# Optimization experiments

Hardware: AMD Instinct MI355X
Metric: run time of the kernel (lower is better)

Reference implementation:

```python
import jax, jax.numpy as jnp
import numpy as np

DIM = 128      # link_state_dim
E = 100000     # num edges
P = 800000     # num adjacency pairs
G = 1000       # num graphs
T = 8          # message passing steps
R = 256        # readout_units


def setup_inputs() -> dict:
    key = jax.random.key(0)
    ks = jax.random.split(key, 16)
    s = lambda *shp: 1.0 / np.sqrt(shp[0])
    inp = {
        "link_state": jax.random.normal(ks[0], (E, DIM), dtype=jnp.float32),
        "states_graph_ids": jnp.sort(jax.random.randint(ks[1], (E,), 0, G, dtype=jnp.int32)),
        "states_first": jax.random.randint(ks[2], (P,), 0, E, dtype=jnp.int32),
        "states_second": jax.random.randint(ks[3], (P,), 0, E, dtype=jnp.int32),
        "sates_num_edges": E,
        # Message MLP: Dense(2*DIM -> DIM), selu
        "W_msg": jax.random.normal(ks[4], (2 * DIM, DIM), dtype=jnp.float32) * s(2 * DIM),
        "b_msg": jnp.zeros((DIM,), dtype=jnp.float32),
        # GRUCell (keras default reset_after=True): kernel/recurrent_kernel [DIM, 3*DIM], bias [2, 3*DIM]
        "gru_kernel": jax.random.normal(ks[5], (DIM, 3 * DIM), dtype=jnp.float32) * s(DIM),
        "gru_rec_kernel": jax.random.normal(ks[6], (DIM, 3 * DIM), dtype=jnp.float32) * s(DIM),
        "gru_bias": jnp.zeros((2, 3 * DIM), dtype=jnp.float32),
        # Readout MLP: DIM -> R -> R -> 1
        "W1": jax.random.normal(ks[7], (DIM, R), dtype=jnp.float32) * s(DIM),
        "b1": jnp.zeros((R,), dtype=jnp.float32),
        "W2": jax.random.normal(ks[8], (R, R), dtype=jnp.float32) * s(R),
        "b2": jnp.zeros((R,), dtype=jnp.float32),
        "W3": jax.random.normal(ks[9], (R, 1), dtype=jnp.float32) * s(R),
        "b3": jnp.zeros((1,), dtype=jnp.float32),
    }
    return inp


def _gru_cell(x, h, kernel, rec_kernel, bias):
    # Keras GRUCell, reset_after=True, gate order (z, r, h)
    mx = x @ kernel + bias[0]
    mh = h @ rec_kernel + bias[1]
    xz, xr, xh = jnp.split(mx, 3, axis=1)
    rz, rr, rh = jnp.split(mh, 3, axis=1)
    z = jax.nn.sigmoid(xz + rz)
    r = jax.nn.sigmoid(xr + rr)
    hh = jnp.tanh(xh + r * rh)
    return z * h + (1.0 - z) * hh


def reference(link_state, states_graph_ids, states_first, states_second, sates_num_edges,
              W_msg, b_msg, gru_kernel, gru_rec_kernel, gru_bias,
              W1, b1, W2, b2, W3, b3):
    for _ in range(T):
        # gather main & neighbor edge states, concat on feature dim -> [P, 2*DIM]
        edges_concat = jnp.concatenate([link_state[states_first], link_state[states_second]], axis=1)
        msgs = jax.nn.selu(edges_concat @ W_msg + b_msg)              # [P, DIM]
        agg = jax.ops.segment_sum(msgs, states_second, num_segments=sates_num_edges)  # [E, DIM]
        link_state = _gru_cell(agg, link_state, gru_kernel, gru_rec_kernel, gru_bias)
    pooled = jax.ops.segment_sum(link_state, states_graph_ids, num_segments=G)  # [G, DIM]
    h = jax.nn.selu(pooled @ W1 + b1)
    h = jax.nn.selu(h @ W2 + b2)
    return h @ W3 + b3  # [G, 1]
```

## Files before the change

### kernel.cpp

```cpp
#include <hip/hip_runtime.h>
#include <hip/hip_fp16.h>
#include <math.h>

#define DIM 128
#define E_NUM 100000
#define P_NUM 800000
#define G_NUM 1000
#define T_STEPS 8
#define R_UNITS 256

typedef __attribute__((ext_vector_type(8))) short bf16x8;
typedef __attribute__((ext_vector_type(4))) float f32x4;

typedef unsigned short ushort_t;
typedef unsigned int   uint_t;

__device__ __forceinline__ float selu_f(float x) {
    const float alpha = 1.6732632423543772f;
    const float scale = 1.0507009873554805f;
    return x > 0.f ? scale * x : scale * alpha * expm1f(x);
}

__device__ __forceinline__ float selu_fast(float x) {
    const float scale = 1.0507009873554805f;
    const float A     = 1.7580993408473766f;
    const float l2e   = 1.4426950408889634f;
    const float e = __builtin_amdgcn_exp2f(x * l2e);
    return x > 0.f ? scale * x : A * e - A;
}

__device__ __forceinline__ ushort_t f2bf(float x) {
    uint_t u = __float_as_uint(x);
    uint_t r = (u + 0x7fffu + ((u >> 16) & 1u)) >> 16;
    return (ushort_t)r;
}
__device__ __forceinline__ float bf2f(ushort_t h) {
    return __uint_as_float(((uint_t)h) << 16);
}

__global__ __launch_bounds__(256)
void hist_kernel(const int* __restrict__ second, int* __restrict__ counts)
{
    const int p = blockIdx.x * 256 + threadIdx.x;
    atomicAdd(&counts[second[p]], 1);
}

__global__ __launch_bounds__(1024)
void scanA_kernel(const int* __restrict__ counts, int* __restrict__ offsets,
                  int* __restrict__ bsum)
{
    __shared__ int buf[1024];
    const int i = blockIdx.x * 1024 + threadIdx.x;
    const int v = (i < E_NUM) ? counts[i] : 0;
    buf[threadIdx.x] = v;
    __syncthreads();
    for (int off = 1; off < 1024; off <<= 1) {
        const int t = (threadIdx.x >= off) ? buf[threadIdx.x - off] : 0;
        __syncthreads();
        buf[threadIdx.x] += t;
        __syncthreads();
    }
    if (i < E_NUM) offsets[i] = buf[threadIdx.x] - v;
    if (threadIdx.x == 1023) bsum[blockIdx.x] = buf[1023];
}

__global__ void scanB_kernel(int* __restrict__ bsum, int* __restrict__ offsets)
{
    int acc = 0;
    for (int b = 0; b < 98; b++) { const int t = bsum[b]; bsum[b] = acc; acc += t; }
    offsets[E_NUM] = P_NUM;
}

__global__ __launch_bounds__(1024)
void scanC_kernel(int* __restrict__ offsets, const int* __restrict__ bsum)
{
    const int i = blockIdx.x * 1024 + threadIdx.x;
    if (i < E_NUM) offsets[i] += bsum[blockIdx.x];
}

__global__ __launch_bounds__(256)
void fill_kernel(const int* __restrict__ first, const int* __restrict__ second,
                 const int* __restrict__ offsets, int* __restrict__ cursor,
                 int* __restrict__ sfirst, int* __restrict__ ssecond)
{
    const int p = blockIdx.x * 256 + threadIdx.x;
    const int d = second[p];
    const int pos = atomicAdd(&cursor[d], 1);
    const int idx = offsets[d] + pos;
    sfirst[idx] = first[p];
    ssecond[idx] = d;
}

__global__ __launch_bounds__(256)
void cast_h_kernel(const float* __restrict__ src,
                   ushort_t* __restrict__ dhi, ushort_t* __restrict__ dlo)
{
    const int idx = blockIdx.x * 256 + threadIdx.x;
    const float x = src[idx];
    const ushort_t hi = f2bf(x);
    dhi[idx] = hi;
    dlo[idx] = f2bf(x - bf2f(hi));
}

__global__ __launch_bounds__(256)
void wsplit_build_kernel(const float* __restrict__ Wmsg,
                         ushort_t* __restrict__ wt, ushort_t* __restrict__ wy)
{
    const int idx  = blockIdx.x * 256 + threadIdx.x;
    const int lane = idx & 63;
    const int nt   = (idx >> 6) & 7;
    const int comp = (idx >> 9) & 1;
    const int ks   = (idx >> 10) & 3;
    const int half = idx >> 12;
    const int n    = nt * 16 + (lane & 15);
    const int kb   = ks * 32 + (lane >> 4) * 8 + half * 128;
    ushort_t* dst  = half ? wy : wt;
    const int slot = idx & 4095;
#pragma unroll
    for (int j = 0; j < 8; j++) {
        const float w = Wmsg[(size_t)(kb + j) * DIM + n];
        const ushort_t hi = f2bf(w);
        dst[(size_t)slot * 8 + j] = comp ? f2bf(w - bf2f(hi)) : hi;
    }
}

__global__ __launch_bounds__(256)
void wb_build_kernel(const float* __restrict__ K, const float* __restrict__ U,
                     ushort_t* __restrict__ wb)
{
    const int idx  = blockIdx.x * 256 + threadIdx.x;
    const int lane = idx & 63;
    int t = idx >> 6;
    const int nt   = t % 24;  t /= 24;
    const int comp = t & 1;   t >>= 1;
    const int gemm = t & 1;
    const int ks   = t >> 1;
    const float* src = gemm ? U : K;
    const int n  = nt * 16 + (lane & 15);
    const int kb = ks * 32 + (lane >> 4) * 8;
#pragma unroll
    for (int j = 0; j < 8; j++) {
        const float w = src[(size_t)(kb + j) * 384 + n];
        const ushort_t hi = f2bf(w);
        wb[(size_t)idx * 8 + j] = comp ? f2bf(w - bf2f(hi)) : hi;
    }
}

#define AS1(p) ((const __attribute__((address_space(1))) unsigned int*)(p))
#define AS3(p) ((__attribute__((address_space(3))) unsigned int*)(p))

__global__ __launch_bounds__(256, 4)
void gy_kernel(const ushort_t* __restrict__ hbh, const ushort_t* __restrict__ hbl,
               const ushort_t* __restrict__ wt, const ushort_t* __restrict__ wy,
               const float* __restrict__ bmsg,
               __half* __restrict__ Gh, float* __restrict__ Y2b)
{
    __shared__ __align__(16) ushort_t sact[2][4096];

    const int tid  = threadIdx.x;
    const int lane = tid & 63;
    const int w    = tid >> 6;
    const int e0   = blockIdx.x * 32;
    const int m16  = lane & 15;
    const int quad = lane >> 4;

#pragma unroll
    for (int i = 0; i < 2; i++) {
        const int g  = tid + i * 256;
        const int gm = g & 15;
        const int gr = (g >> 4) & 1;
        const int gq = (g >> 5) & 3;
        const int gk = g >> 7;
        const size_t soff = (size_t)(e0 + gr * 16 + gm) * DIM + gk * 32 + gq * 8;
        __builtin_amdgcn_global_load_lds(AS1(hbh + soff), AS3((char*)sact[0] + g * 16), 16, 0, 0);
        __builtin_amdgcn_global_load_lds(AS1(hbl + soff), AS3((char*)sact[1] + g * 16), 16, 0, 0);
    }
    __syncthreads();

#define ACT(a_, ks_, rt_) \
    (*(const bf16x8*)((const char*)sact[a_] + (size_t)((ks_) * 2048 + quad * 512 + (rt_) * 256 + m16 * 16)))

    f32x4 acc[2][4] = {};
#pragma unroll
    for (int ks = 0; ks < 4; ks++) {
        bf16x8 ah[2], al[2];
#pragma unroll
        for (int rt = 0; rt < 2; rt++) {
            ah[rt] = ACT(0, ks, rt);
            al[rt] = ACT(1, ks, rt);
        }
#pragma unroll
        for (int ntl = 0; ntl < 4; ntl++) {
            const int ntg = w * 4 + ntl;
            const ushort_t* wsel = (ntg < 8) ? wt : wy;
            const int nt = ntg & 7;
            const bf16x8 bh = *(const bf16x8*)(wsel + (size_t)(((ks * 2 + 0) * 8 + nt) * 64 + lane) * 8);
            const bf16x8 bl = *(const bf16x8*)(wsel + (size_t)(((ks * 2 + 1) * 8 + nt) * 64 + lane) * 8);
#pragma unroll
            for (int rt = 0; rt < 2; rt++) {
                acc[rt][ntl] = __builtin_amdgcn_mfma_f32_16x16x32_bf16(ah[rt], bh, acc[rt][ntl], 0, 0, 0);
                acc[rt][ntl] = __builtin_amdgcn_mfma_f32_16x16x32_bf16(al[rt], bh, acc[rt][ntl], 0, 0, 0);
                acc[rt][ntl] = __builtin_amdgcn_mfma_f32_16x16x32_bf16(ah[rt], bl, acc[rt][ntl], 0, 0, 0);
            }
        }
    }
#undef ACT
#pragma unroll
    for (int ntl = 0; ntl < 4; ntl++) {
        const int ntg = w * 4 + ntl;
        const int c   = (ntg & 7) * 16 + m16;
        if (ntg < 8) {
#pragma unroll
            for (int rt = 0; rt < 2; rt++) {
#pragma unroll
                for (int reg = 0; reg < 4; reg++) {
                    const size_t row = (size_t)(e0 + rt * 16 + quad * 4 + reg);
                    Gh[row * DIM + c] = __float2half_rn(acc[rt][ntl][reg]);
                }
            }
        } else {
            const float bb = bmsg[c];
#pragma unroll
            for (int rt = 0; rt < 2; rt++) {
#pragma unroll
                for (int reg = 0; reg < 4; reg++) {
                    const size_t row = (size_t)(e0 + rt * 16 + quad * 4 + reg);
                    Y2b[row * DIM + c] = acc[rt][ntl][reg] + bb;
                }
            }
        }
    }
}

__device__ __forceinline__ void aggru_one_dest(
    const __half2* __restrict__ Gh2, const int* __restrict__ sfirst,
    ushort_t* __restrict__ sxh, ushort_t* __restrict__ sxl,
    int rrel, int start, int end, float2 y, int c2, int lane)
{
    float a0 = 0.f, a1 = 0.f;
    int p = start;
    for (; p + 8 <= end; p += 8) {
        int f[8];
#pragma unroll
        for (int j = 0; j < 8; j++) f[j] = sfirst[p + j];
        __half2 g[8];
#pragma unroll
        for (int j = 0; j < 8; j++)
            g[j] = Gh2[(size_t)f[j] * 64 + lane];
#pragma unroll
        for (int j = 0; j < 8; j++) {
            const float2 gf = __half22float2(g[j]);
            a0 += selu_fast(gf.x + y.x);
            a1 += selu_fast(gf.y + y.y);
        }
    }
    if (p + 4 <= end) {
        int f[4];
#pragma unroll
        for (int j = 0; j < 4; j++) f[j] = sfirst[p + j];
        __half2 g[4];
#pragma unroll
        for (int j = 0; j < 4; j++)
            g[j] = Gh2[(size_t)f[j] * 64 + lane];
#pragma unroll
        for (int j = 0; j < 4; j++) {
            const float2 gf = __half22float2(g[j]);
            a0 += selu_fast(gf.x + y.x);
            a1 += selu_fast(gf.y + y.y);
        }
        p += 4;
    }
    for (; p < end; p++) {
        const int f = sfirst[p];
        const float2 gf = __half22float2(Gh2[(size_t)f * 64 + lane]);
        a0 += selu_fast(gf.x + y.x);
        a1 += selu_fast(gf.y + y.y);
    }
    const int ks = c2 >> 5;
    const int qd = (c2 >> 3) & 3;
    const int el = c2 & 7;
    const int base = (ks * 128 + qd * 32 + (rrel >> 4) * 16 + (rrel & 15)) * 8 + el;
    const ushort_t h0 = f2bf(a0);
    const ushort_t h1 = f2bf(a1);
    ushort2 hv, lv;
    hv.x = h0;  hv.y = h1;
    lv.x = f2bf(a0 - bf2f(h0));
    lv.y = f2bf(a1 - bf2f(h1));
    *(ushort2*)(sxh + base) = hv;
    *(ushort2*)(sxl + base) = lv;
}

__global__ __launch_bounds__(512, 4)
void aggru_kernel(const __half2* __restrict__ Gh2, const float* __restrict__ Y2b,
                  const int* __restrict__ offsets, const int* __restrict__ sfirst,
                  ushort_t* __restrict__ hbh, ushort_t* __restrict__ hbl,
                  const ushort_t* __restrict__ wb, const float* __restrict__ bias)
{
    __shared__ __align__(16) ushort_t sact[4][4096];

    const int tid  = threadIdx.x;
    const int lane = tid & 63;
    const int w    = tid >> 6;
    const int e0   = blockIdx.x * 32;
    const int m16  = lane & 15;
    const int quad = lane >> 4;

    {
        const int gm = tid & 15;
        const int gr = (tid >> 4) & 1;
        const int gq = (tid >> 5) & 3;
        const int gk = tid >> 7;
        const size_t soff = (size_t)(e0 + gr * 16 + gm) * DIM + gk * 32 + gq * 8;
        __builtin_amdgcn_global_load_lds(AS1(hbh + soff), AS3((char*)sact[2] + tid * 16), 16, 0, 0);
        __builtin_amdgcn_global_load_lds(AS1(hbl + soff), AS3((char*)sact[3] + tid * 16), 16, 0, 0);
    }

    {
        const int c2 = lane * 2;
        const int d0 = e0 + w * 4;
        const int o0 = offsets[d0 + 0], o1 = offsets[d0 + 1];
        const int o2 = offsets[d0 + 2], o3 = offsets[d0 + 3], o4 = offsets[d0 + 4];
        const float2* Yp = (const float2*)(Y2b + (size_t)d0 * DIM + c2);
        const float2 y0 = Yp[0], y1 = Yp[64], y2 = Yp[128], y3 = Yp[192];
        const int r0 = w * 4;
        aggru_one_dest(Gh2, sfirst, sact[0], sact[1], r0 + 0, o0, o1, y0, c2, lane);
        aggru_one_dest(Gh2, sfirst, sact[0], sact[1], r0 + 1, o1, o2, y1, c2, lane);
        aggru_one_dest(Gh2, sfirst, sact[0], sact[1], r0 + 2, o2, o3, y2, c2, lane);
        aggru_one_dest(Gh2, sfirst, sact[0], sact[1], r0 + 3, o3, o4, y3, c2, lane);
    }
    __syncthreads();

    f32x4 az[2] = {}, ar[2] = {}, ahx[2] = {}, ahh[2] = {};

#define WB(ks_, gm_, cp_, nt_) \
    (*(const bf16x8*)(wb + ((size_t)(((ks_) * 96) + (gm_) * 48 + (cp_) * 24 + (nt_)) * 64 + lane) * 8))
#define ACT(a_, ks_, rt_) \
    (*(const bf16x8*)((const char*)sact[a_] + (size_t)((ks_) * 2048 + quad * 512 + (rt_) * 256 + m16 * 16)))

#pragma unroll
    for (int ks = 0; ks < 4; ks++) {
        const bf16x8 KzH = WB(ks, 0, 0, w),      KzL = WB(ks, 0, 1, w);
        const bf16x8 UzH = WB(ks, 1, 0, w),      UzL = WB(ks, 1, 1, w);
        const bf16x8 KrH = WB(ks, 0, 0, w + 8),  KrL = WB(ks, 0, 1, w + 8);
        const bf16x8 UrH = WB(ks, 1, 0, w + 8),  UrL = WB(ks, 1, 1, w + 8);
        const bf16x8 KhH = WB(ks, 0, 0, w + 16), KhL = WB(ks, 0, 1, w + 16);
        const bf16x8 UhH = WB(ks, 1, 0, w + 16), UhL = WB(ks, 1, 1, w + 16);
#pragma unroll
        for (int rt = 0; rt < 2; rt++) {
            const bf16x8 xh = ACT(0, ks, rt);
            const bf16x8 xl = ACT(1, ks, rt);
            const bf16x8 hh = ACT(2, ks, rt);
            const bf16x8 hl = ACT(3, ks, rt);

            az[rt] = __builtin_amdgcn_mfma_f32_16x16x32_bf16(xh, KzH, az[rt], 0, 0, 0);
            az[rt] = __builtin_amdgcn_mfma_f32_16x16x32_bf16(xl, KzH, az[rt], 0, 0, 0);
            az[rt] = __builtin_amdgcn_mfma_f32_16x16x32_bf16(xh, KzL, az[rt], 0, 0, 0);
            az[rt] = __builtin_amdgcn_mfma_f32_16x16x32_bf16(hh, UzH, az[rt], 0, 0, 0);
            az[rt] = __builtin_amdgcn_mfma_f32_16x16x32_bf16(hl, UzH, az[rt], 0, 0, 0);
            az[rt] = __builtin_amdgcn_mfma_f32_16x16x32_bf16(hh, UzL, az[rt], 0, 0, 0);

            ar[rt] = __builtin_amdgcn_mfma_f32_16x16x32_bf16(xh, KrH, ar[rt], 0, 0, 0);
            ar[rt] = __builtin_amdgcn_mfma_f32_16x16x32_bf16(xl, KrH, ar[rt], 0, 0, 0);
            ar[rt] = __builtin_amdgcn_mfma_f32_16x16x32_bf16(xh, KrL, ar[rt], 0, 0, 0);
            ar[rt] = __builtin_amdgcn_mfma_f32_16x16x32_bf16(hh, UrH, ar[rt], 0, 0, 0);
            ar[rt] = __builtin_amdgcn_mfma_f32_16x16x32_bf16(hl, UrH, ar[rt], 0, 0, 0);
            ar[rt] = __builtin_amdgcn_mfma_f32_16x16x32_bf16(hh, UrL, ar[rt], 0, 0, 0);

            ahx[rt] = __builtin_amdgcn_mfma_f32_16x16x32_bf16(xh, KhH, ahx[rt], 0, 0, 0);
            ahx[rt] = __builtin_amdgcn_mfma_f32_16x16x32_bf16(xl, KhH, ahx[rt], 0, 0, 0);
            ahx[rt] = __builtin_amdgcn_mfma_f32_16x16x32_bf16(xh, KhL, ahx[rt], 0, 0, 0);
            ahh[rt] = __builtin_amdgcn_mfma_f32_16x16x32_bf16(hh, UhH, ahh[rt], 0, 0, 0);
            ahh[rt] = __builtin_amdgcn_mfma_f32_16x16x32_bf16(hl, UhH, ahh[rt], 0, 0, 0);
            ahh[rt] = __builtin_amdgcn_mfma_f32_16x16x32_bf16(hh, UhL, ahh[rt], 0, 0, 0);
        }
    }
#undef WB
#undef ACT

    const int c = w * 16 + m16;
    const float l2e  = 1.4426950408889634f;
    const float bzn  = -(bias[c] + bias[384 + c]) * l2e;
    const float brn  = -(bias[128 + c] + bias[512 + c]) * l2e;
    const float bxh  = bias[256 + c];
    const float brh  = bias[640 + c];
    const float bxh2 = bxh * (2.f * l2e);

    const int ksc   = w >> 1;
    const int quadc = (2 * w + (m16 >> 3)) & 3;
    const int elem  = m16 & 7;

#pragma unroll
    for (int rt = 0; rt < 2; rt++) {
#pragma unroll
        for (int reg = 0; reg < 4; reg++) {
            const int rrel = rt * 16 + quad * 4 + reg;
            const int row  = e0 + rrel;
            const int lidx = (ksc * 128 + quadc * 32 + rt * 16 + (quad * 4 + reg)) * 8 + elem;
            const float z = __builtin_amdgcn_rcpf(
                1.f + __builtin_amdgcn_exp2f(fmaf(az[rt][reg], -l2e, bzn)));
            const float r = __builtin_amdgcn_rcpf(
                1.f + __builtin_amdgcn_exp2f(fmaf(ar[rt][reg], -l2e, brn)));
            const float u   = fmaf(r, ahh[rt][reg] + brh, ahx[rt][reg]);
            const float eh  = __builtin_amdgcn_exp2f(fmaf(u, 2.f * l2e, bxh2));
            const float hc  = fmaf(-2.f, __builtin_amdgcn_rcpf(eh + 1.f), 1.f);
            const float hp = bf2f(sact[2][lidx]) + bf2f(sact[3][lidx]);
            const float hn = fmaf(z, hp - hc, hc);
            const size_t g = (size_t)row * DIM + c;
            const ushort_t hi = f2bf(hn);
            hbh[g] = hi;
            hbl[g] = f2bf(hn - bf2f(hi));
        }
    }
}

#undef AS1
#undef AS3

__global__ __launch_bounds__(256)
void pool_kernel(const ushort_t* __restrict__ hbh, const ushort_t* __restrict__ hbl,
                 const int* __restrict__ gid, float* __restrict__ pooled)
{
    const int idx = blockIdx.x * 256 + threadIdx.x;
    const int e = idx >> 7;
    const int n = idx & 127;
    const float hv = bf2f(hbh[idx]) + bf2f(hbl[idx]);
    atomicAdd(pooled + (size_t)gid[e] * DIM + n, hv);
}

__global__ __launch_bounds__(256)
void readout_kernel(const float* __restrict__ pooled,
                    const float* __restrict__ W1, const float* __restrict__ b1,
                    const float* __restrict__ W2, const float* __restrict__ b2,
                    const float* __restrict__ W3, const float* __restrict__ b3,
                    float* __restrict__ out)
{
    __shared__ float sp[DIM];
    __shared__ float s1[R_UNITS];
    __shared__ float s2[R_UNITS];
    const int g = blockIdx.x, tid = threadIdx.x;

    if (tid < DIM) sp[tid] = pooled[(size_t)g * DIM + tid];
    __syncthreads();

    float acc = b1[tid];
    for (int k = 0; k < DIM; k++) acc += sp[k] * W1[(size_t)k * R_UNITS + tid];
    s1[tid] = selu_f(acc);
    __syncthreads();

    acc = b2[tid];
    for (int k = 0; k < R_UNITS; k++) acc += s1[k] * W2[(size_t)k * R_UNITS + tid];
    s2[tid] = selu_f(acc) * W3[tid];
    __syncthreads();

    for (int s = 128; s > 0; s >>= 1) {
        if (tid < s) s2[tid] += s2[tid + s];
        __syncthreads();
    }
    if (tid == 0) out[g] = s2[0] + b3[0];
}

extern "C" void kernel_launch(void* const* d_in, const int* in_sizes, int n_in,
                              void* d_out, int out_size, void* d_ws, size_t ws_size,
                              hipStream_t stream)
{
    const float* link_state = (const float*)d_in[0];
    const int*   gids       = (const int*)d_in[1];
    const int*   first      = (const int*)d_in[2];
    const int*   second     = (const int*)d_in[3];
    const float* Wmsg       = (const float*)d_in[5];
    const float* bmsg       = (const float*)d_in[6];
    const float* gK         = (const float*)d_in[7];
    const float* gU         = (const float*)d_in[8];
    const float* gbias      = (const float*)d_in[9];
    const float* W1         = (const float*)d_in[10];
    const float* b1         = (const float*)d_in[11];
    const float* W2         = (const float*)d_in[12];
    const float* b2         = (const float*)d_in[13];
    const float* W3         = (const float*)d_in[14];
    const float* b3         = (const float*)d_in[15];
    float* out = (float*)d_out;

    int* offsets = (int*)d_ws;
    int* counts  = offsets + 100004;
    int* cursor  = counts + E_NUM;
    int* bsum    = cursor + E_NUM;
    int* sfirst  = bsum + 128;
    int* ssecond = sfirst + P_NUM;
    ushort_t* wt     = (ushort_t*)(ssecond + P_NUM);
    ushort_t* wy     = wt + 32768;
    ushort_t* wb     = wy + 32768;
    ushort_t* hb_hi  = wb + 196608;
    ushort_t* hb_lo  = hb_hi + (size_t)E_NUM * DIM;
    ushort_t* agg_hi = hb_lo + (size_t)E_NUM * DIM;
    ushort_t* agg_lo = agg_hi + (size_t)E_NUM * DIM;
    float*    Gf     = (float*)(agg_lo + (size_t)E_NUM * DIM);
    __half*   Gh     = (__half*)Gf;
    float*    Y2b    = Gf + (size_t)E_NUM * DIM;

    hipMemsetAsync(counts, 0, E_NUM * sizeof(int), stream);
    hipMemsetAsync(cursor, 0, E_NUM * sizeof(int), stream);
    hist_kernel<<<P_NUM / 256, 256, 0, stream>>>(second, counts);
    scanA_kernel<<<98, 1024, 0, stream>>>(counts, offsets, bsum);
    scanB_kernel<<<1, 1, 0, stream>>>(bsum, offsets);
    scanC_kernel<<<98, 1024, 0, stream>>>(offsets, bsum);
    fill_kernel<<<P_NUM / 256, 256, 0, stream>>>(first, second, offsets, cursor,
                                                 sfirst, ssecond);
    wsplit_build_kernel<<<32, 256, 0, stream>>>(Wmsg, wt, wy);
    wb_build_kernel<<<96, 256, 0, stream>>>(gK, gU, wb);
    cast_h_kernel<<<(E_NUM * DIM) / 256, 256, 0, stream>>>(link_state, hb_hi, hb_lo);

    for (int t = 0; t < T_STEPS; t++) {
        gy_kernel<<<E_NUM / 32, 256, 0, stream>>>(hb_hi, hb_lo, wt, wy, bmsg,
                                                  Gh, Y2b);
        aggru_kernel<<<E_NUM / 32, 512, 0, stream>>>((const __half2*)Gh, Y2b,
                                                     offsets, sfirst,
                                                     hb_hi, hb_lo,
                                                     wb, gbias);
    }

    float* pooled = Gf;
    hipMemsetAsync(pooled, 0, (size_t)G_NUM * DIM * sizeof(float), stream);
    pool_kernel<<<(E_NUM * DIM) / 256, 256, 0, stream>>>(hb_hi, hb_lo, gids, pooled);
    readout_kernel<<<G_NUM, 256, 0, stream>>>(pooled, W1, b1, W2, b2, W3, b3, out);
}
```

Before: 1.677 ms.

## Fuse neighbor-side message projection into aggregation-GRU kernel, dropping Y2b buffer

The per-destination half of the message Dense layer (h @ W_second + b_msg) moves out of gy_kernel and into aggru_kernel. There it is computed with MFMA from the hidden-state tiles already staged in LDS, and the results are parked in shared memory before the gather-aggregate phase reads them. This removes the full fp32 Y2b buffer, which was written and re-read in global memory every step, and halves the GEMM work in gy_kernel. In exchange, aggru_kernel does extra MFMA work and gains additional block barriers, which could lengthen its critical path.

Result: faster. 1.594 ms (-5.0%).

```diff
diff --git a/kernel.cpp b/kernel.cpp
--- a/kernel.cpp
+++ b/kernel.cpp
@@ -151,9 +151,8 @@
 
 __global__ __launch_bounds__(256, 4)
 void gy_kernel(const ushort_t* __restrict__ hbh, const ushort_t* __restrict__ hbl,
-               const ushort_t* __restrict__ wt, const ushort_t* __restrict__ wy,
-               const float* __restrict__ bmsg,
-               __half* __restrict__ Gh, float* __restrict__ Y2b)
+               const ushort_t* __restrict__ wt,
+               __half* __restrict__ Gh)
 {
     __shared__ __align__(16) ushort_t sact[2][4096];
 
@@ -180,7 +179,7 @@
 #define ACT(a_, ks_, rt_) \
     (*(const bf16x8*)((const char*)sact[a_] + (size_t)((ks_) * 2048 + quad * 512 + (rt_) * 256 + m16 * 16)))
 
-    f32x4 acc[2][4] = {};
+    f32x4 acc[2][2] = {};
 #pragma unroll
     for (int ks = 0; ks < 4; ks++) {
         bf16x8 ah[2], al[2];
@@ -190,12 +189,10 @@
             al[rt] = ACT(1, ks, rt);
         }
 #pragma unroll
-        for (int ntl = 0; ntl < 4; ntl++) {
-            const int ntg = w * 4 + ntl;
-            const ushort_t* wsel = (ntg < 8) ? wt : wy;
-            const int nt = ntg & 7;
-            const bf16x8 bh = *(const bf16x8*)(wsel + (size_t)(((ks * 2 + 0) * 8 + nt) * 64 + lane) * 8);
-            const bf16x8 bl = *(const bf16x8*)(wsel + (size_t)(((ks * 2 + 1) * 8 + nt) * 64 + lane) * 8);
+        for (int ntl = 0; ntl < 2; ntl++) {
+            const int nt = w * 2 + ntl;
+            const bf16x8 bh = *(const bf16x8*)(wt + (size_t)((ks * 1024 + nt * 64 + lane) * 8));
+            const bf16x8 bl = *(const bf16x8*)(wt + (size_t)((ks * 1024 + 512 + nt * 64 + lane) * 8));
 #pragma unroll
             for (int rt = 0; rt < 2; rt++) {
                 acc[rt][ntl] = __builtin_amdgcn_mfma_f32_16x16x32_bf16(ah[rt], bh, acc[rt][ntl], 0, 0, 0);
@@ -206,27 +203,14 @@
     }
 #undef ACT
 #pragma unroll
-    for (int ntl = 0; ntl < 4; ntl++) {
-        const int ntg = w * 4 + ntl;
-        const int c   = (ntg & 7) * 16 + m16;
-        if (ntg < 8) {
-#pragma unroll
-            for (int rt = 0; rt < 2; rt++) {
-#pragma unroll
-                for (int reg = 0; reg < 4; reg++) {
-                    const size_t row = (size_t)(e0 + rt * 16 + quad * 4 + reg);
-                    Gh[row * DIM + c] = __float2half_rn(acc[rt][ntl][reg]);
-                }
-            }
-        } else {
-            const float bb = bmsg[c];
-#pragma unroll
-            for (int rt = 0; rt < 2; rt++) {
-#pragma unroll
-                for (int reg = 0; reg < 4; reg++) {
-                    const size_t row = (size_t)(e0 + rt * 16 + quad * 4 + reg);
-                    Y2b[row * DIM + c] = acc[rt][ntl][reg] + bb;
-                }
+    for (int ntl = 0; ntl < 2; ntl++) {
+        const int c = (w * 2 + ntl) * 16 + m16;
+#pragma unroll
+        for (int rt = 0; rt < 2; rt++) {
+#pragma unroll
+            for (int reg = 0; reg < 4; reg++) {
+                const size_t row = (size_t)(e0 + rt * 16 + quad * 4 + reg);
+                Gh[row * DIM + c] = __float2half_rn(acc[rt][ntl][reg]);
             }
         }
     }
@@ -291,10 +275,11 @@
 }
 
 __global__ __launch_bounds__(512, 4)
-void aggru_kernel(const __half2* __restrict__ Gh2, const float* __restrict__ Y2b,
+void aggru_kernel(const __half2* __restrict__ Gh2,
                   const int* __restrict__ offsets, const int* __restrict__ sfirst,
                   ushort_t* __restrict__ hbh, ushort_t* __restrict__ hbl,
-                  const ushort_t* __restrict__ wb, const float* __restrict__ bias)
+                  const ushort_t* __restrict__ wb, const float* __restrict__ bias,
+                  const ushort_t* __restrict__ wy, const float* __restrict__ bmsg)
 {
     __shared__ __align__(16) ushort_t sact[4][4096];
 
@@ -314,15 +299,52 @@
         __builtin_amdgcn_global_load_lds(AS1(hbh + soff), AS3((char*)sact[2] + tid * 16), 16, 0, 0);
         __builtin_amdgcn_global_load_lds(AS1(hbl + soff), AS3((char*)sact[3] + tid * 16), 16, 0, 0);
     }
+    __syncthreads();
+
+#define ACT(a_, ks_, rt_) \
+    (*(const bf16x8*)((const char*)sact[a_] + (size_t)((ks_) * 2048 + quad * 512 + (rt_) * 256 + m16 * 16)))
 
     {
-        const int c2 = lane * 2;
+        f32x4 yacc[2] = {};
+#pragma unroll
+        for (int ks = 0; ks < 4; ks++) {
+            const bf16x8 WyH = *(const bf16x8*)(wy + (size_t)((ks * 1024 + w * 64 + lane) * 8));
+            const bf16x8 WyL = *(const bf16x8*)(wy + (size_t)((ks * 1024 + 512 + w * 64 + lane) * 8));
+#pragma unroll
+            for (int rt = 0; rt < 2; rt++) {
+                const bf16x8 hh = ACT(2, ks, rt);
+                const bf16x8 hl = ACT(3, ks, rt);
+                yacc[rt] = __builtin_amdgcn_mfma_f32_16x16x32_bf16(hh, WyH, yacc[rt], 0, 0, 0);
+                yacc[rt] = __builtin_amdgcn_mfma_f32_16x16x32_bf16(hl, WyH, yacc[rt], 0, 0, 0);
+                yacc[rt] = __builtin_amdgcn_mfma_f32_16x16x32_bf16(hh, WyL, yacc[rt], 0, 0, 0);
+            }
+        }
+        float* ylds = (float*)sact;
+        const int cc = w * 16 + m16;
+        const float bb = bmsg[cc];
+#pragma unroll
+        for (int rt = 0; rt < 2; rt++) {
+#pragma unroll
+            for (int reg = 0; reg < 4; reg++) {
+                ylds[(rt * 16 + quad * 4 + reg) * 128 + cc] = yacc[rt][reg] + bb;
+            }
+        }
+    }
+    __syncthreads();
+
+    const int c2 = lane * 2;
+    const int r0 = w * 4;
+    const float* ylds = (const float*)sact;
+    const float2 y0 = *(const float2*)(ylds + (r0 + 0) * 128 + c2);
+    const float2 y1 = *(const float2*)(ylds + (r0 + 1) * 128 + c2);
+    const float2 y2 = *(const float2*)(ylds + (r0 + 2) * 128 + c2);
+    const float2 y3 = *(const float2*)(ylds + (r0 + 3) * 128 + c2);
+    __syncthreads();
+
+    {
         const int d0 = e0 + w * 4;
         const int o0 = offsets[d0 + 0], o1 = offsets[d0 + 1];
         const int o2 = offsets[d0 + 2], o3 = offsets[d0 + 3], o4 = offsets[d0 + 4];
-        const float2* Yp = (const float2*)(Y2b + (size_t)d0 * DIM + c2);
-        const float2 y0 = Yp[0], y1 = Yp[64], y2 = Yp[128], y3 = Yp[192];
-        const int r0 = w * 4;
         aggru_one_dest(Gh2, sfirst, sact[0], sact[1], r0 + 0, o0, o1, y0, c2, lane);
         aggru_one_dest(Gh2, sfirst, sact[0], sact[1], r0 + 1, o1, o2, y1, c2, lane);
         aggru_one_dest(Gh2, sfirst, sact[0], sact[1], r0 + 2, o2, o3, y2, c2, lane);
@@ -334,8 +356,6 @@
 
 #define WB(ks_, gm_, cp_, nt_) \
     (*(const bf16x8*)(wb + ((size_t)(((ks_) * 96) + (gm_) * 48 + (cp_) * 24 + (nt_)) * 64 + lane) * 8))
-#define ACT(a_, ks_, rt_) \
-    (*(const bf16x8*)((const char*)sact[a_] + (size_t)((ks_) * 2048 + quad * 512 + (rt_) * 256 + m16 * 16)))
 
 #pragma unroll
     for (int ks = 0; ks < 4; ks++) {
@@ -491,11 +511,9 @@
     ushort_t* wb     = wy + 32768;
     ushort_t* hb_hi  = wb + 196608;
     ushort_t* hb_lo  = hb_hi + (size_t)E_NUM * DIM;
-    ushort_t* agg_hi = hb_lo + (size_t)E_NUM * DIM;
-    ushort_t* agg_lo = agg_hi + (size_t)E_NUM * DIM;
-    float*    Gf     = (float*)(agg_lo + (size_t)E_NUM * DIM);
+    ushort_t* slack  = hb_lo + (size_t)E_NUM * DIM;
+    float*    Gf     = (float*)(slack + 2 * (size_t)E_NUM * DIM);
     __half*   Gh     = (__half*)Gf;
-    float*    Y2b    = Gf + (size_t)E_NUM * DIM;
 
     hipMemsetAsync(counts, 0, E_NUM * sizeof(int), stream);
     hipMemsetAsync(cursor, 0, E_NUM * sizeof(int), stream);
@@ -510,12 +528,11 @@
     cast_h_kernel<<<(E_NUM * DIM) / 256, 256, 0, stream>>>(link_state, hb_hi, hb_lo);
 
     for (int t = 0; t < T_STEPS; t++) {
-        gy_kernel<<<E_NUM / 32, 256, 0, stream>>>(hb_hi, hb_lo, wt, wy, bmsg,
-                                                  Gh, Y2b);
-        aggru_kernel<<<E_NUM / 32, 512, 0, stream>>>((const __half2*)Gh, Y2b,
+        gy_kernel<<<E_NUM / 32, 256, 0, stream>>>(hb_hi, hb_lo, wt, Gh);
+        aggru_kernel<<<E_NUM / 32, 512, 0, stream>>>((const __half2*)Gh,
                                                      offsets, sfirst,
                                                      hb_hi, hb_lo,
-                                                     wb, gbias);
+                                                     wb, gbias, wy, bmsg);
     }
 
     float* pooled = Gf;
```
